# Optimization experiments

Hardware: AMD Instinct MI355X
Metric: run time of the kernel (lower is better)

Reference implementation:

```python
import jax, jax.numpy as jnp
import numpy as np

N_NODES = 100000
N_EDGES = 1600000
D_IN = 128
HIDDEN = 128
EPS = 1e-5


def setup_inputs() -> dict:
    key = jax.random.key(0)
    ks = jax.random.split(key, 12)
    glorot = lambda k, o, i: jax.random.normal(k, (o, i), jnp.float32) * (2.0 / (o + i)) ** 0.5
    return {
        "x": jax.random.normal(ks[0], (N_NODES, D_IN), jnp.float32),
        "edge_index": jax.random.randint(ks[1], (2, N_EDGES), 0, N_NODES, jnp.int64),
        # SAGEConv layer 1: lin_l (neighbors, with bias), lin_r (root, no bias)
        "Wl1": glorot(ks[2], HIDDEN, D_IN),
        "bl1": jnp.zeros((HIDDEN,), jnp.float32),
        "Wr1": glorot(ks[3], HIDDEN, D_IN),
        # SAGEConv layer 2
        "Wl2": glorot(ks[4], HIDDEN, HIDDEN),
        "bl2": jnp.zeros((HIDDEN,), jnp.float32),
        "Wr2": glorot(ks[5], HIDDEN, HIDDEN),
        # BatchNorm1d affine params
        "gamma": jnp.ones((HIDDEN,), jnp.float32),
        "beta": jnp.zeros((HIDDEN,), jnp.float32),
        # final fc (xavier_uniform weight, zero bias per init_weights)
        "fcW": jax.random.uniform(ks[6], (HIDDEN, HIDDEN), jnp.float32, -1.0, 1.0) * (6.0 / (2 * HIDDEN)) ** 0.5,
        "fcb": jnp.zeros((HIDDEN,), jnp.float32),
    }


def _sage_conv(h, src, dst, n, Wl, bl, Wr):
    # mean-aggregate neighbor features: scatter x[src] onto dst
    msg_sum = jax.ops.segment_sum(h[src], dst, num_segments=n)          # [N, F]
    deg = jax.ops.segment_sum(jnp.ones((src.shape[0],), h.dtype), dst, num_segments=n)
    agg = msg_sum / jnp.maximum(deg, 1.0)[:, None]
    return agg @ Wl.T + bl + h @ Wr.T


def reference(x, edge_index, Wl1, bl1, Wr1, Wl2, bl2, Wr2, gamma, beta, fcW, fcb):
    src, dst = edge_index[0], edge_index[1]
    n = x.shape[0]
    h = jax.nn.relu(_sage_conv(x, src, dst, n, Wl1, bl1, Wr1))  # inter-layer relu in PyG BasicGNN
    h = _sage_conv(h, src, dst, n, Wl2, bl2, Wr2)
    h = jax.nn.relu(h)
    # BatchNorm1d, training-mode (batch stats, biased variance)
    mu = h.mean(axis=0)
    var = ((h - mu) ** 2).mean(axis=0)
    h = (h - mu) * jax.lax.rsqrt(var + EPS) * gamma + beta
    # dropout p=0.0 -> identity
    return h @ fcW.T + fcb
```

## Files before the change

kernel.cpp:

```cpp
#include <hip/hip_runtime.h>
#include <hip/hip_bf16.h>

#define D 128
#define EPSV 1e-5f
#define BSH 7
#define BWIDTH 128
#define NCB 256
#define MAXBUCK 1024

typedef __attribute__((ext_vector_type(8))) short bf16x8;
typedef __attribute__((ext_vector_type(4))) float f32x4;
typedef unsigned short u16;

__device__ inline u16 f2bf(float f) {
    unsigned int u = __builtin_bit_cast(unsigned int, f);
    return (u16)((u + 0x7fffu + ((u >> 16) & 1u)) >> 16);
}
__device__ inline float bf2f(u16 u) {
    unsigned int x = ((unsigned int)u) << 16;
    return __builtin_bit_cast(float, x);
}

__global__ void k_cvt(const float* __restrict__ in, u16* __restrict__ out, long long n8) {
    long long i = (long long)blockIdx.x * blockDim.x + threadIdx.x;
    long long stride = (long long)gridDim.x * blockDim.x;
    for (; i < n8; i += stride) {
        const float4 v0 = *(const float4*)(in + i * 8);
        const float4 v1 = *(const float4*)(in + i * 8 + 4);
        bf16x8 o;
        o[0] = (short)f2bf(v0.x); o[1] = (short)f2bf(v0.y);
        o[2] = (short)f2bf(v0.z); o[3] = (short)f2bf(v0.w);
        o[4] = (short)f2bf(v1.x); o[5] = (short)f2bf(v1.y);
        o[6] = (short)f2bf(v1.z); o[7] = (short)f2bf(v1.w);
        *(bf16x8*)(out + i * 8) = o;
    }
}

__global__ __launch_bounds__(256) void k_cvt4(const float* __restrict__ s0, const float* __restrict__ s1,
                                              const float* __restrict__ s2, const float* __restrict__ s3,
                                              u16* __restrict__ out) {
    int i = blockIdx.x * 256 + threadIdx.x;
    int mat = i >> 11;
    int off = (i & 2047) * 8;
    const float* src = (mat == 0) ? s0 : (mat == 1) ? s1 : (mat == 2) ? s2 : s3;
    const float4 v0 = *(const float4*)(src + off);
    const float4 v1 = *(const float4*)(src + off + 4);
    bf16x8 o;
    o[0] = (short)f2bf(v0.x); o[1] = (short)f2bf(v0.y);
    o[2] = (short)f2bf(v0.z); o[3] = (short)f2bf(v0.w);
    o[4] = (short)f2bf(v1.x); o[5] = (short)f2bf(v1.y);
    o[6] = (short)f2bf(v1.z); o[7] = (short)f2bf(v1.w);
    *(bf16x8*)(out + (size_t)i * 8) = o;
}

__global__ __launch_bounds__(256) void k_bhist(const int* __restrict__ dst, int E, int chunk,
                                               int nbuck, int* __restrict__ bh) {
    __shared__ int h[MAXBUCK];
    int t = threadIdx.x;
    for (int i = t; i < nbuck; i += 256) h[i] = 0;
    __syncthreads();
    int beg = blockIdx.x * chunk, end = min(E, beg + chunk);
    for (int i = beg + t; i < end; i += 256) atomicAdd(&h[dst[i] >> BSH], 1);
    __syncthreads();
    for (int i = t; i < nbuck; i += 256) bh[(size_t)blockIdx.x * nbuck + i] = h[i];
}

__global__ __launch_bounds__(NCB) void k_colscan(int* __restrict__ bh, int nbuck, int* __restrict__ btot) {
    __shared__ int sm[NCB];
    int b = blockIdx.x;
    int t = threadIdx.x;
    int v = bh[(size_t)t * nbuck + b];
    sm[t] = v;
    __syncthreads();
    for (int off = 1; off < NCB; off <<= 1) {
        int a = (t >= off) ? sm[t - off] : 0;
        __syncthreads();
        sm[t] += a;
        __syncthreads();
    }
    bh[(size_t)t * nbuck + b] = sm[t] - v;
    if (t == NCB - 1) btot[b] = sm[t];
}

__global__ __launch_bounds__(1024) void k_btotscan(const int* __restrict__ btot, int nbuck,
                                                   int* __restrict__ bbase, int* __restrict__ row_ptr,
                                                   int M, int E) {
    __shared__ int sm[1024];
    int t = threadIdx.x;
    int v = (t < nbuck) ? btot[t] : 0;
    sm[t] = v;
    __syncthreads();
    for (int off = 1; off < 1024; off <<= 1) {
        int a = (t >= off) ? sm[t - off] : 0;
        __syncthreads();
        sm[t] += a;
        __syncthreads();
    }
    if (t < nbuck) bbase[t] = sm[t] - v;
    if (t == 0) { bbase[nbuck] = E; row_ptr[M] = E; }
}

__global__ __launch_bounds__(256) void k_bfill(const int* __restrict__ src, const int* __restrict__ dst,
                                               int E, int chunk, int nbuck, const int* __restrict__ bh,
                                               const int* __restrict__ bbase, unsigned int* __restrict__ pairs) {
    __shared__ int cur[MAXBUCK];
    int t = threadIdx.x;
    for (int i = t; i < nbuck; i += 256)
        cur[i] = bbase[i] + bh[(size_t)blockIdx.x * nbuck + i];
    __syncthreads();
    int beg = blockIdx.x * chunk, end = min(E, beg + chunk);
    for (int i = beg + t; i < end; i += 256) {
        int d = dst[i];
        int bk = d >> BSH;
        int pos = atomicAdd(&cur[bk], 1);
        pairs[pos] = (unsigned int)src[i] | ((unsigned int)(d & (BWIDTH - 1)) << 24);
    }
}

__global__ __launch_bounds__(256) void k_b2csr(const unsigned int* __restrict__ pairs,
                                               const int* __restrict__ bbase, int nbuck, int M,
                                               int* __restrict__ row_ptr, int* __restrict__ csr) {
    __shared__ int nh[BWIDTH];
    __shared__ int sc[BWIDTH];
    __shared__ int nc[BWIDTH];
    int b = blockIdx.x;
    int t = threadIdx.x;
    int node0 = b << BSH;
    int beg = bbase[b], end = bbase[b + 1];
    if (t < BWIDTH) nh[t] = 0;
    __syncthreads();
    for (int i = beg + t; i < end; i += 256) atomicAdd(&nh[pairs[i] >> 24], 1);
    __syncthreads();
    if (t < BWIDTH) sc[t] = nh[t];
    __syncthreads();
    for (int off = 1; off < BWIDTH; off <<= 1) {
        int a = 0;
        if (t < BWIDTH && t >= off) a = sc[t - off];
        __syncthreads();
        if (t < BWIDTH) sc[t] += a;
        __syncthreads();
    }
    if (t < BWIDTH) {
        int ex = sc[t] - nh[t];
        nc[t] = ex;
        int node = node0 + t;
        if (node < M) row_ptr[node] = beg + ex;
    }
    __syncthreads();
    for (int i = beg + t; i < end; i += 256) {
        unsigned int p = pairs[i];
        int pos = atomicAdd(&nc[p >> 24], 1);
        csr[beg + pos] = (int)(p & 0xFFFFFFu);
    }
}

__global__ __launch_bounds__(256) void k_gather(const u16* __restrict__ feat, const int* __restrict__ rp,
                                                const int* __restrict__ csr, u16* __restrict__ msg, int M) {
    int sub = threadIdx.x & 15;
    int node = blockIdx.x * 16 + (threadIdx.x >> 4);
    if (node >= M) return;
    int beg = rp[node], end = rp[node + 1];
    float a0[8], a1[8], a2[8], a3[8];
    #pragma unroll
    for (int j = 0; j < 8; j++) { a0[j] = 0.f; a1[j] = 0.f; a2[j] = 0.f; a3[j] = 0.f; }
    int e = beg;
    for (; e + 3 < end; e += 4) {
        int s0 = csr[e], s1 = csr[e + 1], s2 = csr[e + 2], s3 = csr[e + 3];
        bf16x8 v0 = *(const bf16x8*)(feat + (size_t)s0 * D + sub * 8);
        bf16x8 v1 = *(const bf16x8*)(feat + (size_t)s1 * D + sub * 8);
        bf16x8 v2 = *(const bf16x8*)(feat + (size_t)s2 * D + sub * 8);
        bf16x8 v3 = *(const bf16x8*)(feat + (size_t)s3 * D + sub * 8);
        #pragma unroll
        for (int j = 0; j < 8; j++) {
            a0[j] += bf2f((u16)v0[j]);
            a1[j] += bf2f((u16)v1[j]);
            a2[j] += bf2f((u16)v2[j]);
            a3[j] += bf2f((u16)v3[j]);
        }
    }
    for (; e < end; e++) {
        bf16x8 v0 = *(const bf16x8*)(feat + (size_t)csr[e] * D + sub * 8);
        #pragma unroll
        for (int j = 0; j < 8; j++) a0[j] += bf2f((u16)v0[j]);
    }
    float inv = 1.0f / fmaxf((float)(end - beg), 1.0f);
    bf16x8 o;
    #pragma unroll
    for (int j = 0; j < 8; j++) o[j] = (short)f2bf((a0[j] + a1[j] + a2[j] + a3[j]) * inv);
    *(bf16x8*)(msg + (size_t)node * D + sub * 8) = o;
}

template <int TWO, int RELU, int OUTBF>
__global__ __launch_bounds__(256) void k_gemm(
    const u16* __restrict__ A1, const u16* __restrict__ A2,
    const u16* __restrict__ W1b, const u16* __restrict__ W2b,
    const float* __restrict__ bias, void* __restrict__ Cout,
    int M, int nstrips) {
    __shared__ u16 wlds[(TWO ? 2 : 1) * 16384];
    int t = threadIdx.x;
    {
        const int nrows = TWO ? 256 : 128;
        for (int idx = t; idx < nrows; idx += 256) {
            int mat = idx >> 7, row = idx & 127;
            const u16* g = (mat ? W2b : W1b) + (size_t)row * D;
            u16* base = wlds + mat * 16384 + row * D;
            #pragma unroll
            for (int c16 = 0; c16 < 16; c16++) {
                bf16x8 v = *(const bf16x8*)(g + c16 * 8);
                *(bf16x8*)(base + ((c16 ^ (row & 7)) * 8)) = v;
            }
        }
    }
    __syncthreads();

    int lane = t & 63, wave = t >> 6;
    int rlo = lane & 15, khi = lane >> 4;

    for (int s = blockIdx.x; s < nstrips; s += gridDim.x) {
        int m0 = s * 128 + wave * 32;
        bf16x8 a1f[2][4], a2f[2][4];
        #pragma unroll
        for (int mt = 0; mt < 2; mt++) {
            int ra = m0 + mt * 16 + rlo;
            if (ra > M - 1) ra = M - 1;
            const u16* ar = A1 + (size_t)ra * D;
            #pragma unroll
            for (int kk = 0; kk < 4; kk++)
                a1f[mt][kk] = *(const bf16x8*)(ar + kk * 32 + khi * 8);
            if (TWO) {
                const u16* ar2 = A2 + (size_t)ra * D;
                #pragma unroll
                for (int kk = 0; kk < 4; kk++)
                    a2f[mt][kk] = *(const bf16x8*)(ar2 + kk * 32 + khi * 8);
            }
        }

        f32x4 acc[2][8];
        #pragma unroll
        for (int mt = 0; mt < 2; mt++)
            #pragma unroll
            for (int nt = 0; nt < 8; nt++) acc[mt][nt] = (f32x4){0.f, 0.f, 0.f, 0.f};

        #pragma unroll
        for (int nt = 0; nt < 8; nt++) {
            int row = nt * 16 + rlo;
            const u16* wb = wlds + (size_t)row * D;
            bf16x8 wf[4];
            #pragma unroll
            for (int kk = 0; kk < 4; kk++)
                wf[kk] = *(const bf16x8*)(wb + ((kk * 4 + khi) ^ (row & 7)) * 8);
            #pragma unroll
            for (int mt = 0; mt < 2; mt++)
                #pragma unroll
                for (int kk = 0; kk < 4; kk++)
                    acc[mt][nt] = __builtin_amdgcn_mfma_f32_16x16x32_bf16(a1f[mt][kk], wf[kk], acc[mt][nt], 0, 0, 0);
            if (TWO) {
                const u16* wb2 = wlds + 16384 + (size_t)row * D;
                bf16x8 wf2[4];
                #pragma unroll
                for (int kk = 0; kk < 4; kk++)
                    wf2[kk] = *(const bf16x8*)(wb2 + ((kk * 4 + khi) ^ (row & 7)) * 8);
                #pragma unroll
                for (int mt = 0; mt < 2; mt++)
                    #pragma unroll
                    for (int kk = 0; kk < 4; kk++)
                        acc[mt][nt] = __builtin_amdgcn_mfma_f32_16x16x32_bf16(a2f[mt][kk], wf2[kk], acc[mt][nt], 0, 0, 0);
            }
        }

        #pragma unroll
        for (int mt = 0; mt < 2; mt++)
            #pragma unroll
            for (int nt = 0; nt < 8; nt++) {
                int col = nt * 16 + rlo;
                float bn = bias[col];
                #pragma unroll
                for (int r = 0; r < 4; r++) {
                    int row = m0 + mt * 16 + khi * 4 + r;
                    if (row < M) {
                        float v = acc[mt][nt][r] + bn;
                        if (RELU) v = fmaxf(v, 0.0f);
                        if (OUTBF) ((u16*)Cout)[(size_t)row * D + col] = f2bf(v);
                        else       ((float*)Cout)[(size_t)row * D + col] = v;
                    }
                }
            }
    }
}

__global__ __launch_bounds__(256) void k_bnstats(const u16* __restrict__ h, int M, float* __restrict__ stats) {
    __shared__ float ssum[256];
    __shared__ float ssq[256];
    int col = threadIdx.x & 127;
    int half = threadIdx.x >> 7;
    float s = 0.f, s2 = 0.f;
    for (int r = blockIdx.x * 2 + half; r < M; r += 512) {
        float v = bf2f(h[(size_t)r * D + col]);
        s += v;
        s2 += v * v;
    }
    ssum[threadIdx.x] = s;
    ssq[threadIdx.x] = s2;
    __syncthreads();
    if (threadIdx.x < 128) {
        unsafeAtomicAdd(&stats[col], ssum[threadIdx.x] + ssum[threadIdx.x + 128]);
        unsafeAtomicAdd(&stats[128 + col], ssq[threadIdx.x] + ssq[threadIdx.x + 128]);
    }
}

__global__ __launch_bounds__(128) void k_bnfold(const float* __restrict__ stats,
                                                const float* __restrict__ gamma, const float* __restrict__ beta,
                                                const float* __restrict__ fcW, const float* __restrict__ fcb,
                                                int M, u16* __restrict__ Wfold, float* __restrict__ bias2) {
    __shared__ float red[128];
    int n = blockIdx.x, t = threadIdx.x;
    float mu = stats[t] / (float)M;
    float var = stats[128 + t] / (float)M - mu * mu;
    float sc = gamma[t] * rsqrtf(var + EPSV);
    float sh = beta[t] - mu * sc;
    float w = fcW[(size_t)n * D + t];
    Wfold[(size_t)n * D + t] = f2bf(w * sc);
    red[t] = sh * w;
    __syncthreads();
    for (int off = 64; off > 0; off >>= 1) {
        if (t < off) red[t] += red[t + off];
        __syncthreads();
    }
    if (t == 0) bias2[n] = fcb[n] + red[0];
}

static inline size_t alup(size_t x) { return (x + 63) & ~(size_t)63; }

extern "C" void kernel_launch(void* const* d_in, const int* in_sizes, int n_in,
                              void* d_out, int out_size, void* d_ws, size_t ws_size,
                              hipStream_t stream) {
    const float* x   = (const float*)d_in[0];
    const int*   ei  = (const int*)d_in[1];
    const float* Wl1 = (const float*)d_in[2];
    const float* bl1 = (const float*)d_in[3];
    const float* Wr1 = (const float*)d_in[4];
    const float* Wl2 = (const float*)d_in[5];
    const float* bl2 = (const float*)d_in[6];
    const float* Wr2 = (const float*)d_in[7];
    const float* gamma = (const float*)d_in[8];
    const float* beta  = (const float*)d_in[9];
    const float* fcW = (const float*)d_in[10];
    const float* fcb = (const float*)d_in[11];
    float* out = (float*)d_out;

    const int M = in_sizes[0] / D;
    const int E = in_sizes[1] / 2;
    const int* srcI = ei;
    const int* dstI = ei + E;
    const int nbuck = (M + BWIDTH - 1) >> BSH;
    const int chunk = (E + NCB - 1) / NCB;

    char* p = (char*)d_ws;
    u16* xb   = (u16*)p;            p += alup((size_t)M * D * 2);
    u16* msgb = (u16*)p;            p += alup((size_t)M * D * 2);
    u16* h1b  = (u16*)p;            p += alup((size_t)M * D * 2);
    u16* h2b  = (u16*)p;            p += alup((size_t)M * D * 2);
    unsigned int* pairs = (unsigned int*)p; p += alup((size_t)E * 4);
    int* csr  = (int*)p;            p += alup((size_t)E * 4);
    int* row_ptr = (int*)p;         p += alup((size_t)(M + 1) * 4);
    int* bh   = (int*)p;            p += alup((size_t)NCB * nbuck * 4);
    int* btot = (int*)p;            p += alup((size_t)nbuck * 4);
    int* bbase= (int*)p;            p += alup((size_t)(nbuck + 1) * 4);
    float* stats = (float*)p;       p += alup(256 * 4);
    u16* Wb   = (u16*)p;            p += alup((size_t)4 * D * D * 2);
    u16* Wfoldb = (u16*)p;          p += alup((size_t)D * D * 2);
    float* bias2 = (float*)p;       p += alup(128 * 4);

    u16* Wl1b = Wb;
    u16* Wr1b = Wb + 16384;
    u16* Wl2b = Wb + 32768;
    u16* Wr2b = Wb + 49152;

    const int nstrips = (M + 127) / 128;
    const int GG = nstrips < 512 ? nstrips : 512;
    const int gather_grid = (M + 15) / 16;

    hipMemsetAsync(stats, 0, 256 * sizeof(float), stream);

    k_cvt<<<2048, 256, 0, stream>>>(x, xb, (long long)M * D / 8);
    k_cvt4<<<32, 256, 0, stream>>>(Wl1, Wr1, Wl2, Wr2, Wb);
    k_bhist<<<NCB, 256, 0, stream>>>(dstI, E, chunk, nbuck, bh);
    k_colscan<<<nbuck, NCB, 0, stream>>>(bh, nbuck, btot);
    k_btotscan<<<1, 1024, 0, stream>>>(btot, nbuck, bbase, row_ptr, M, E);
    k_bfill<<<NCB, 256, 0, stream>>>(srcI, dstI, E, chunk, nbuck, bh, bbase, pairs);
    k_b2csr<<<nbuck, 256, 0, stream>>>(pairs, bbase, nbuck, M, row_ptr, csr);

    k_gather<<<gather_grid, 256, 0, stream>>>(xb, row_ptr, csr, msgb, M);
    k_gemm<1, 1, 1><<<GG, 256, 0, stream>>>(msgb, xb, Wl1b, Wr1b, bl1, h1b, M, nstrips);

    k_gather<<<gather_grid, 256, 0, stream>>>(h1b, row_ptr, csr, msgb, M);
    k_gemm<1, 1, 1><<<GG, 256, 0, stream>>>(msgb, h1b, Wl2b, Wr2b, bl2, h2b, M, nstrips);

    k_bnstats<<<256, 256, 0, stream>>>(h2b, M, stats);
    k_bnfold<<<128, 128, 0, stream>>>(stats, gamma, beta, fcW, fcb, M, Wfoldb, bias2);

    k_gemm<0, 0, 0><<<GG, 256, 0, stream>>>(h2b, nullptr, Wfoldb, nullptr, bias2, out, M, nstrips);
}
```

Baseline: 451.5 us.

## Double-buffer GEMM A-tiles via global_load_lds and unroll gather by eight

```diff
diff --git a/kernel.cpp b/kernel.cpp
--- a/kernel.cpp
+++ b/kernel.cpp
@@ -19,6 +19,13 @@
 __device__ inline float bf2f(u16 u) {
     unsigned int x = ((unsigned int)u) << 16;
     return __builtin_bit_cast(float, x);
+}
+
+__device__ inline void gl_lds16(const void* g, void* l) {
+    __builtin_amdgcn_global_load_lds(
+        (const __attribute__((address_space(1))) unsigned int*)g,
+        (__attribute__((address_space(3))) unsigned int*)l,
+        16, 0, 0);
 }
 
 __global__ void k_cvt(const float* __restrict__ in, u16* __restrict__ out, long long n8) {
@@ -164,6 +171,25 @@
     #pragma unroll
     for (int j = 0; j < 8; j++) { a0[j] = 0.f; a1[j] = 0.f; a2[j] = 0.f; a3[j] = 0.f; }
     int e = beg;
+    for (; e + 7 < end; e += 8) {
+        int s0 = csr[e], s1 = csr[e + 1], s2 = csr[e + 2], s3 = csr[e + 3];
+        int s4 = csr[e + 4], s5 = csr[e + 5], s6 = csr[e + 6], s7 = csr[e + 7];
+        bf16x8 v0 = *(const bf16x8*)(feat + (size_t)s0 * D + sub * 8);
+        bf16x8 v1 = *(const bf16x8*)(feat + (size_t)s1 * D + sub * 8);
+        bf16x8 v2 = *(const bf16x8*)(feat + (size_t)s2 * D + sub * 8);
+        bf16x8 v3 = *(const bf16x8*)(feat + (size_t)s3 * D + sub * 8);
+        bf16x8 v4 = *(const bf16x8*)(feat + (size_t)s4 * D + sub * 8);
+        bf16x8 v5 = *(const bf16x8*)(feat + (size_t)s5 * D + sub * 8);
+        bf16x8 v6 = *(const bf16x8*)(feat + (size_t)s6 * D + sub * 8);
+        bf16x8 v7 = *(const bf16x8*)(feat + (size_t)s7 * D + sub * 8);
+        #pragma unroll
+        for (int j = 0; j < 8; j++) {
+            a0[j] += bf2f((u16)v0[j]); a1[j] += bf2f((u16)v1[j]);
+            a2[j] += bf2f((u16)v2[j]); a3[j] += bf2f((u16)v3[j]);
+            a0[j] += bf2f((u16)v4[j]); a1[j] += bf2f((u16)v5[j]);
+            a2[j] += bf2f((u16)v6[j]); a3[j] += bf2f((u16)v7[j]);
+        }
+    }
     for (; e + 3 < end; e += 4) {
         int s0 = csr[e], s1 = csr[e + 1], s2 = csr[e + 2], s3 = csr[e + 3];
         bf16x8 v0 = *(const bf16x8*)(feat + (size_t)s0 * D + sub * 8);
@@ -172,10 +198,8 @@
         bf16x8 v3 = *(const bf16x8*)(feat + (size_t)s3 * D + sub * 8);
         #pragma unroll
         for (int j = 0; j < 8; j++) {
-            a0[j] += bf2f((u16)v0[j]);
-            a1[j] += bf2f((u16)v1[j]);
-            a2[j] += bf2f((u16)v2[j]);
-            a3[j] += bf2f((u16)v3[j]);
+            a0[j] += bf2f((u16)v0[j]); a1[j] += bf2f((u16)v1[j]);
+            a2[j] += bf2f((u16)v2[j]); a3[j] += bf2f((u16)v3[j]);
         }
     }
     for (; e < end; e++) {
@@ -196,10 +220,37 @@
     const u16* __restrict__ W1b, const u16* __restrict__ W2b,
     const float* __restrict__ bias, void* __restrict__ Cout,
     int M, int nstrips) {
-    __shared__ u16 wlds[(TWO ? 2 : 1) * 16384];
-    int t = threadIdx.x;
+    constexpr int NOPS = TWO ? 2 : 1;
+    __shared__ __align__(16) u16 lds[NOPS * 16384 + 2 * NOPS * 8192];
+    u16* wlds = lds;
+    u16* alds = lds + NOPS * 16384;
+
+    int t = threadIdx.x;
+    int lane = t & 63, wave = t >> 6;
+    int rlo = lane & 15, khi = lane >> 4;
+
+    auto stage = [&](int buf, int sidx) {
+        int rsub = khi;
+        #pragma unroll
+        for (int c = 0; c < 4; c++) {
+            int chunk = wave * 4 + c;
+            int lrow = chunk * 4 + rsub;
+            int ra = sidx * 64 + lrow;
+            if (ra > M - 1) ra = M - 1;
+            int src16 = rlo ^ (lrow & 7);
+            gl_lds16(A1 + (size_t)ra * D + src16 * 8,
+                     alds + ((size_t)buf * NOPS + 0) * 8192 + chunk * 512);
+            if (TWO)
+                gl_lds16(A2 + (size_t)ra * D + src16 * 8,
+                         alds + ((size_t)buf * NOPS + 1) * 8192 + chunk * 512);
+        }
+    };
+
+    int s0 = blockIdx.x;
+    if (s0 < nstrips) stage(0, s0);
+
     {
-        const int nrows = TWO ? 256 : 128;
+        const int nrows = NOPS * 128;
         for (int idx = t; idx < nrows; idx += 256) {
             int mat = idx >> 7, row = idx & 127;
             const u16* g = (mat ? W2b : W1b) + (size_t)row * D;
@@ -213,78 +264,61 @@
     }
     __syncthreads();
 
-    int lane = t & 63, wave = t >> 6;
-    int rlo = lane & 15, khi = lane >> 4;
-
-    for (int s = blockIdx.x; s < nstrips; s += gridDim.x) {
-        int m0 = s * 128 + wave * 32;
-        bf16x8 a1f[2][4], a2f[2][4];
-        #pragma unroll
-        for (int mt = 0; mt < 2; mt++) {
-            int ra = m0 + mt * 16 + rlo;
-            if (ra > M - 1) ra = M - 1;
-            const u16* ar = A1 + (size_t)ra * D;
+    int cur = 0;
+    for (int s = s0; s < nstrips; s += gridDim.x) {
+        int nxt = s + gridDim.x;
+        if (nxt < nstrips) stage(cur ^ 1, nxt);
+
+        int r_local = wave * 16 + rlo;
+        bf16x8 af[NOPS][4];
+        #pragma unroll
+        for (int o = 0; o < NOPS; o++) {
+            const u16* ab = alds + ((size_t)cur * NOPS + o) * 8192 + r_local * D;
             #pragma unroll
             for (int kk = 0; kk < 4; kk++)
-                a1f[mt][kk] = *(const bf16x8*)(ar + kk * 32 + khi * 8);
-            if (TWO) {
-                const u16* ar2 = A2 + (size_t)ra * D;
+                af[o][kk] = *(const bf16x8*)(ab + (((kk * 4 + khi) ^ (r_local & 7)) * 8));
+        }
+
+        f32x4 acc[8];
+        #pragma unroll
+        for (int nt = 0; nt < 8; nt++) acc[nt] = (f32x4){0.f, 0.f, 0.f, 0.f};
+
+        #pragma unroll
+        for (int nt = 0; nt < 8; nt++) {
+            int row = nt * 16 + rlo;
+            #pragma unroll
+            for (int o = 0; o < NOPS; o++) {
+                const u16* wb = wlds + o * 16384 + (size_t)row * D;
+                bf16x8 wf[4];
                 #pragma unroll
                 for (int kk = 0; kk < 4; kk++)
-                    a2f[mt][kk] = *(const bf16x8*)(ar2 + kk * 32 + khi * 8);
-            }
-        }
-
-        f32x4 acc[2][8];
-        #pragma unroll
-        for (int mt = 0; mt < 2; mt++)
-            #pragma unroll
-            for (int nt = 0; nt < 8; nt++) acc[mt][nt] = (f32x4){0.f, 0.f, 0.f, 0.f};
-
-        #pragma unroll
-        for (int nt = 0; nt < 8; nt++) {
-            int row = nt * 16 + rlo;
-            const u16* wb = wlds + (size_t)row * D;
-            bf16x8 wf[4];
-            #pragma unroll
-            for (int kk = 0; kk < 4; kk++)
-                wf[kk] = *(const bf16x8*)(wb + ((kk * 4 + khi) ^ (row & 7)) * 8);
-            #pragma unroll
-            for (int mt = 0; mt < 2; mt++)
+                    wf[kk] = *(const bf16x8*)(wb + (((kk * 4 + khi) ^ (row & 7)) * 8));
                 #pragma unroll
                 for (int kk = 0; kk < 4; kk++)
-                    acc[mt][nt] = __builtin_amdgcn_mfma_f32_16x16x32_bf16(a1f[mt][kk], wf[kk], acc[mt][nt], 0, 0, 0);
-            if (TWO) {
-                const u16* wb2 = wlds + 16384 + (size_t)row * D;
-                bf16x8 wf2[4];
-                #pragma unroll
-                for (int kk = 0; kk < 4; kk++)
-                    wf2[kk] = *(const bf16x8*)(wb2 + ((kk * 4 + khi) ^ (row & 7)) * 8);
-                #pragma unroll
-                for (int mt = 0; mt < 2; mt++)
-                    #pragma unroll
-                    for (int kk = 0; kk < 4; kk++)
-                        acc[mt][nt] = __builtin_amdgcn_mfma_f32_16x16x32_bf16(a2f[mt][kk], wf2[kk], acc[mt][nt], 0, 0, 0);
+                    acc[nt] = __builtin_amdgcn_mfma_f32_16x16x32_bf16(af[o][kk], wf[kk], acc[nt], 0, 0, 0);
             }
         }
 
-        #pragma unroll
-        for (int mt = 0; mt < 2; mt++)
+        int mrow0 = s * 64 + wave * 16 + khi * 4;
+        #pragma unroll
+        for (int nt = 0; nt < 8; nt++) {
+            int col = nt * 16 + rlo;
+            float bn = bias[col];
             #pragma unroll
-            for (int nt = 0; nt < 8; nt++) {
-                int col = nt * 16 + rlo;
-                float bn = bias[col];
-                #pragma unroll
-                for (int r = 0; r < 4; r++) {
-                    int row = m0 + mt * 16 + khi * 4 + r;
-                    if (row < M) {
-                        float v = acc[mt][nt][r] + bn;
-                        if (RELU) v = fmaxf(v, 0.0f);
-                        if (OUTBF) ((u16*)Cout)[(size_t)row * D + col] = f2bf(v);
-                        else       ((float*)Cout)[(size_t)row * D + col] = v;
-                    }
+            for (int r = 0; r < 4; r++) {
+                int row = mrow0 + r;
+                if (row < M) {
+                    float v = acc[nt][r] + bn;
+                    if (RELU) v = fmaxf(v, 0.0f);
+                    if (OUTBF) ((u16*)Cout)[(size_t)row * D + col] = f2bf(v);
+                    else       ((float*)Cout)[(size_t)row * D + col] = v;
                 }
             }
+        }
+
+        asm volatile("s_waitcnt vmcnt(32)" ::: "memory");
+        __syncthreads();
+        cur ^= 1;
     }
 }
 
@@ -376,8 +410,9 @@
     u16* Wl2b = Wb + 32768;
     u16* Wr2b = Wb + 49152;
 
-    const int nstrips = (M + 127) / 128;
-    const int GG = nstrips < 512 ? nstrips : 512;
+    const int nstrips = (M + 63) / 64;
+    const int GG2 = 256;
+    const int GG1 = 512;
     const int gather_grid = (M + 15) / 16;
 
     hipMemsetAsync(stats, 0, 256 * sizeof(float), stream);
@@ -391,13 +426,13 @@
     k_b2csr<<<nbuck, 256, 0, stream>>>(pairs, bbase, nbuck, M, row_ptr, csr);
 
     k_gather<<<gather_grid, 256, 0, stream>>>(xb, row_ptr, csr, msgb, M);
-    k_gemm<1, 1, 1><<<GG, 256, 0, stream>>>(msgb, xb, Wl1b, Wr1b, bl1, h1b, M, nstrips);
+    k_gemm<1, 1, 1><<<GG2, 256, 0, stream>>>(msgb, xb, Wl1b, Wr1b, bl1, h1b, M, nstrips);
 
     k_gather<<<gather_grid, 256, 0, stream>>>(h1b, row_ptr, csr, msgb, M);
-    k_gemm<1, 1, 1><<<GG, 256, 0, stream>>>(msgb, h1b, Wl2b, Wr2b, bl2, h2b, M, nstrips);
+    k_gemm<1, 1, 1><<<GG2, 256, 0, stream>>>(msgb, h1b, Wl2b, Wr2b, bl2, h2b, M, nstrips);
 
     k_bnstats<<<256, 256, 0, stream>>>(h2b, M, stats);
     k_bnfold<<<128, 128, 0, stream>>>(stats, gamma, beta, fcW, fcb, M, Wfoldb, bias2);
 
-    k_gemm<0, 0, 0><<<GG, 256, 0, stream>>>(h2b, nullptr, Wfoldb, nullptr, bias2, out, M, nstrips);
-}
+    k_gemm<0, 0, 0><<<GG1, 256, 0, stream>>>(h2b, nullptr, Wfoldb, nullptr, bias2, out, M, nstrips);
+}
```

New measurement: 436.3 us. 3.4% less time.
